# Kernel tuning notes

Measured on AMD Instinct MI355X. Metric: run time of the kernel, lower is better.

The kernel has to match this reference:

```python
import jax, jax.numpy as jnp
import numpy as np

N = 24  # input_size
TRIL = N * (N + 1) // 2  # 300
_rows, _cols = np.tril_indices(N)  # row-major order, matches torch.tril_indices


def setup_inputs() -> dict:
    key = jax.random.key(0)
    ks = jax.random.split(key, 8)
    B = 131072
    x = jax.random.normal(ks[0], (B, N), dtype=jnp.float32)
    # MLP params: Linear(N,128), Linear(128,32), Linear(32,TRIL)
    def lin(k, fan_in, fan_out):
        k1, k2 = jax.random.split(k)
        lim = 1.0 / np.sqrt(fan_in)
        W = jax.random.uniform(k1, (fan_out, fan_in), jnp.float32, -lim, lim)
        b = jax.random.uniform(k2, (fan_out,), jnp.float32, -lim, lim)
        return W, b
    W1, b1 = lin(ks[1], N, 128)
    W2, b2 = lin(ks[2], 128, 32)
    W3, b3 = lin(ks[3], 32, TRIL)
    return {"x": x, "W1": W1, "b1": b1, "W2": W2, "b2": b2, "W3": W3, "b3": b3}


def reference(x, W1, b1, W2, b2, W3, b3):
    # MLP: Linear -> ELU -> Linear -> ELU -> Linear -> Softplus
    h = jax.nn.elu(x @ W1.T + b1)           # [B,128]
    h = jax.nn.elu(h @ W2.T + b2)           # [B,32]
    c = jax.nn.softplus(h @ W3.T + b3)      # [B,TRIL]
    B = x.shape[0]
    # scatter into lower-triangular Cholesky factor
    L = jnp.zeros((B, N, N), dtype=x.dtype).at[:, _rows, _cols].set(c)  # [B,N,N]
    A = jnp.einsum('bij,bkj->bik', L, L)    # C @ C^T, SPD
    y = jnp.einsum('bi,bij,bj->b', x, A, x)[:, None]  # quadratic form, [B,1]
    return y
```

## Files before the change

### kernel.cpp

```cpp
#include <hip/hip_runtime.h>
#include <hip/hip_bf16.h>
#include <math.h>


constexpr int NI  = 24;
constexpr int H1  = 128;
constexpr int H2  = 32;
constexpr int SPB = 128;
constexpr int NT_TOT = 19;
constexpr int W3R = 304;
constexpr float LOG2E = 1.4426950408889634f;
constexpr float LN2SQ = 0.4804530139182014f;

typedef __attribute__((ext_vector_type(8))) short bf16x8;
typedef __attribute__((ext_vector_type(4))) float f32x4;

__device__ __forceinline__ float elu_f(float v) {
    return v > 0.0f ? v : __expf(v) - 1.0f;
}
__device__ __forceinline__ float exp2_hw(float x) {
    float r; asm("v_exp_f32 %0, %1" : "=v"(r) : "v"(x)); return r;
}
__device__ __forceinline__ float log2_hw(float x) {
    float r; asm("v_log_f32 %0, %1" : "=v"(r) : "v"(x)); return r;
}
__device__ __forceinline__ float softplus_g(float zp) {
    return fmaxf(zp, 0.0f) + log2_hw(1.0f + exp2_hw(-fabsf(zp)));
}
__device__ __forceinline__ unsigned short f2bf(float f) {
    return __builtin_bit_cast(unsigned short, __float2bfloat16(f));
}
__device__ __forceinline__ unsigned int pk2(float a, float b) {
    return (unsigned int)f2bf(a) | ((unsigned int)f2bf(b) << 16);
}

__global__ void wcvt(const float* __restrict__ W1, const float* __restrict__ W2,
                     const float* __restrict__ W3, const float* __restrict__ b3,
                     unsigned short* __restrict__ ws) {
    int idx = blockIdx.x * 256 + threadIdx.x;
    if (idx < 4096) {
        int n = idx >> 5, k = idx & 31;
        ws[idx] = f2bf(k < NI ? W1[n * NI + k] : 0.0f);
    } else if (idx < 8192) {
        ws[idx] = f2bf(W2[idx - 4096]);
    } else if (idx < 8192 + W3R * H2) {
        int j = idx - 8192;
        int t = j >> 5;
        ws[idx] = f2bf(t < 300 ? W3[j] * LOG2E : 0.0f);
    } else if (idx < 8192 + W3R * H2 + W3R) {
        int t = idx - (8192 + W3R * H2);
        float* b3s = reinterpret_cast<float*>(ws + 17920);
        b3s[t] = (t < 300) ? b3[t] * LOG2E : 0.0f;
    }
}

template<int J0, int C0>
__device__ __forceinline__ void vaccum(const float xr[NI], float v[12],
                                       const float* __restrict__ crow) {
    #pragma unroll
    for (int q = 0; q < 12; ++q) {
        const int j = 2 * q + J0;
        #pragma unroll
        for (int i = j; i < NI; ++i) {
            const int t = i * (i + 1) / 2 + j;
            if (t >= C0 && t < C0 + 32)
                v[q] = fmaf(xr[i], crow[t - C0], v[q]);
        }
    }
}

template<int CH>
__device__ __forceinline__ void chunk_body(
    int w_hi, int w_lo, int lr, int lq, int sid, int half,
    const unsigned short* __restrict__ w3b, const float* __restrict__ b3s,
    const float xr[NI], float v[12],
    float* __restrict__ c_buf, const unsigned short* __restrict__ h2b)
{
    const int my_nt = 2 * CH + w_hi;
    if (my_nt < NT_TOT) {
        const int t = my_nt * 16 + lr;
        bf16x8 wf = *reinterpret_cast<const bf16x8*>(w3b + t * H2 + lq * 8);
        const float bias = b3s[t];
        #pragma unroll
        for (int q = 0; q < 4; ++q) {
            const int st = 4 * w_lo + q;
            bf16x8 hb = *reinterpret_cast<const bf16x8*>(h2b + (st * 16 + lr) * 40 + lq * 8);
            f32x4 a = {0.f, 0.f, 0.f, 0.f};
            a = __builtin_amdgcn_mfma_f32_16x16x32_bf16(hb, wf, a, 0, 0, 0);
            #pragma unroll
            for (int r = 0; r < 4; ++r) {
                float g = softplus_g(a[r] + bias);
                c_buf[(st * 16 + 4 * lq + r) * 33 + (my_nt & 1) * 16 + lr] = g;
            }
        }
    }
    __syncthreads();
    if (half == 0) vaccum<1, CH * 32>(xr, v, c_buf + sid * 33);
    else           vaccum<0, CH * 32>(xr, v, c_buf + sid * 33);
    __syncthreads();
}

__global__ __launch_bounds__(256, 4) void qnet_fused(
    const float* __restrict__ x,
    const unsigned short* __restrict__ w1b, const float* __restrict__ b1,
    const unsigned short* __restrict__ w2b, const float* __restrict__ b2,
    const unsigned short* __restrict__ w3b, const float* __restrict__ b3s,
    float* __restrict__ y, int B)
{
    __shared__ __align__(16) unsigned char L[30720];
    unsigned short* xb  = reinterpret_cast<unsigned short*>(L);
    unsigned short* h1s = reinterpret_cast<unsigned short*>(L + 10240);
    unsigned short* h2b = reinterpret_cast<unsigned short*>(L + 20480);
    float* c_buf = reinterpret_cast<float*>(L);
    float* yb    = reinterpret_cast<float*>(L + 16896);

    const int tid  = threadIdx.x;
    const int sid  = tid & (SPB - 1);
    const int lane = tid & 63;
    const int lr   = lane & 15, lq = lane >> 4;
    const int half = __builtin_amdgcn_readfirstlane(tid >> 7);
    const int wid  = __builtin_amdgcn_readfirstlane(tid >> 6);
    const int w_hi = wid >> 1, w_lo = wid & 1;
    const size_t sbase = (size_t)blockIdx.x * SPB;

    float xr[NI];
    {
        const float4* xp4 = reinterpret_cast<const float4*>(x + (sbase + sid) * NI);
        #pragma unroll
        for (int q = 0; q < NI / 4; ++q) {
            float4 t4 = xp4[q];
            xr[4*q+0] = t4.x; xr[4*q+1] = t4.y; xr[4*q+2] = t4.z; xr[4*q+3] = t4.w;
        }
    }
    if (half == 0) {
        unsigned int pk[12];
        #pragma unroll
        for (int q = 0; q < 12; ++q) pk[q] = pk2(xr[2*q], xr[2*q+1]);
        uint4* dst = reinterpret_cast<uint4*>(xb + sid * 40);
        dst[0] = make_uint4(pk[0], pk[1], pk[2], pk[3]);
        dst[1] = make_uint4(pk[4], pk[5], pk[6], pk[7]);
        dst[2] = make_uint4(pk[8], pk[9], pk[10], pk[11]);
    } else {
        *reinterpret_cast<uint4*>(xb + sid * 40 + 24) = make_uint4(0, 0, 0, 0);
    }
    __syncthreads();

    f32x4 acc[2][2];
    #pragma unroll
    for (int u = 0; u < 2; ++u)
        #pragma unroll
        for (int n2 = 0; n2 < 2; ++n2) acc[u][n2] = (f32x4){0.f, 0.f, 0.f, 0.f};

    #pragma unroll
    for (int kk = 0; kk < 4; ++kk) {
        const int nt1 = 2 * kk + w_hi;
        bf16x8 af = *reinterpret_cast<const bf16x8*>(w1b + (nt1 * 16 + lr) * 32 + lq * 8);
        const float4 bb1 = *reinterpret_cast<const float4*>(b1 + nt1 * 16 + 4 * lq);
        #pragma unroll
        for (int q = 0; q < 4; ++q) {
            const int st = 4 * w_lo + q;
            bf16x8 bf = *reinterpret_cast<const bf16x8*>(xb + (st * 16 + lr) * 40 + lq * 8);
            f32x4 a = {0.f, 0.f, 0.f, 0.f};
            a = __builtin_amdgcn_mfma_f32_16x16x32_bf16(af, bf, a, 0, 0, 0);
            unsigned int p0 = pk2(elu_f(a[0] + bb1.x), elu_f(a[1] + bb1.y));
            unsigned int p1 = pk2(elu_f(a[2] + bb1.z), elu_f(a[3] + bb1.w));
            unsigned long long pw = (unsigned long long)p0 | ((unsigned long long)p1 << 32);
            *reinterpret_cast<unsigned long long*>(
                h1s + (st * 16 + lr) * 40 + w_hi * 16 + 4 * lq) = pw;
        }
        __syncthreads();
        #pragma unroll
        for (int u = 0; u < 2; ++u) {
            const int st2 = 2 * wid + u;
            bf16x8 hb = *reinterpret_cast<const bf16x8*>(h1s + (st2 * 16 + lr) * 40 + lq * 8);
            #pragma unroll
            for (int n2 = 0; n2 < 2; ++n2) {
                bf16x8 wf = *reinterpret_cast<const bf16x8*>(
                    w2b + (n2 * 16 + lr) * H1 + kk * 32 + lq * 8);
                acc[u][n2] = __builtin_amdgcn_mfma_f32_16x16x32_bf16(wf, hb, acc[u][n2], 0, 0, 0);
            }
        }
        __syncthreads();
    }

    #pragma unroll
    for (int u = 0; u < 2; ++u) {
        const int st2 = 2 * wid + u;
        #pragma unroll
        for (int n2 = 0; n2 < 2; ++n2) {
            const float4 bb2 = *reinterpret_cast<const float4*>(b2 + n2 * 16 + 4 * lq);
            unsigned int p0 = pk2(elu_f(acc[u][n2][0] + bb2.x), elu_f(acc[u][n2][1] + bb2.y));
            unsigned int p1 = pk2(elu_f(acc[u][n2][2] + bb2.z), elu_f(acc[u][n2][3] + bb2.w));
            unsigned long long pw = (unsigned long long)p0 | ((unsigned long long)p1 << 32);
            *reinterpret_cast<unsigned long long*>(
                h2b + (st2 * 16 + lr) * 40 + n2 * 16 + 4 * lq) = pw;
        }
    }
    __syncthreads();

    float v[12];
    #pragma unroll
    for (int q = 0; q < 12; ++q) v[q] = 0.f;

    chunk_body<0>(w_hi, w_lo, lr, lq, sid, half, w3b, b3s, xr, v, c_buf, h2b);
    chunk_body<1>(w_hi, w_lo, lr, lq, sid, half, w3b, b3s, xr, v, c_buf, h2b);
    chunk_body<2>(w_hi, w_lo, lr, lq, sid, half, w3b, b3s, xr, v, c_buf, h2b);
    chunk_body<3>(w_hi, w_lo, lr, lq, sid, half, w3b, b3s, xr, v, c_buf, h2b);
    chunk_body<4>(w_hi, w_lo, lr, lq, sid, half, w3b, b3s, xr, v, c_buf, h2b);
    chunk_body<5>(w_hi, w_lo, lr, lq, sid, half, w3b, b3s, xr, v, c_buf, h2b);
    chunk_body<6>(w_hi, w_lo, lr, lq, sid, half, w3b, b3s, xr, v, c_buf, h2b);
    chunk_body<7>(w_hi, w_lo, lr, lq, sid, half, w3b, b3s, xr, v, c_buf, h2b);
    chunk_body<8>(w_hi, w_lo, lr, lq, sid, half, w3b, b3s, xr, v, c_buf, h2b);
    chunk_body<9>(w_hi, w_lo, lr, lq, sid, half, w3b, b3s, xr, v, c_buf, h2b);

    float acc_y = 0.f;
    #pragma unroll
    for (int q = 0; q < 12; ++q) acc_y = fmaf(v[q], v[q], acc_y);

    if (half == 1) yb[sid] = acc_y;
    __syncthreads();
    if (half == 0) y[sbase + sid] = LN2SQ * (acc_y + yb[sid]);
}

extern "C" void kernel_launch(void* const* d_in, const int* in_sizes, int n_in,
                              void* d_out, int out_size, void* d_ws, size_t ws_size,
                              hipStream_t stream) {
    const float* x  = (const float*)d_in[0];
    const float* W1 = (const float*)d_in[1];
    const float* b1 = (const float*)d_in[2];
    const float* W2 = (const float*)d_in[3];
    const float* b2 = (const float*)d_in[4];
    const float* W3 = (const float*)d_in[5];
    const float* b3 = (const float*)d_in[6];
    float* y = (float*)d_out;

    unsigned short* ws = (unsigned short*)d_ws;
    const unsigned short* w1b = ws;
    const unsigned short* w2b = ws + 4096;
    const unsigned short* w3b = ws + 8192;
    const float* b3s = reinterpret_cast<const float*>(ws + 17920);

    const int B = in_sizes[0] / NI;
    const int cvt_elems = 8192 + W3R * H2 + W3R;
    wcvt<<<dim3((cvt_elems + 255) / 256), dim3(256), 0, stream>>>(W1, W2, W3, b3, ws);
    qnet_fused<<<dim3(B / SPB), dim3(256), 0, stream>>>(
        x, w1b, b1, w2b, b2, w3b, b3s, y, B);
}
```

Baseline: 35.62 us.

## Split triangle consumption by element halves and vectorize c_buf stores and loads

Swaps the MFMA operand order so each lane holds four consecutive triangle outputs, which can be written to LDS as one 16-byte vector into a row stride of 36 instead of four scalar stores at stride 33. The two thread halves now split each 32-entry chunk by element (16 each) rather than by odd/even column j. Each half keeps a full 24-wide v accumulator, and the halves combine the vectors through LDS before squaring. This aims to cut LDS instruction count and balance the FMA work between halves, at the cost of more registers for v and a larger final reduction exchange.

Measured after the change: 38.70 us. 8.7% more time.

```diff
diff --git a/kernel.cpp b/kernel.cpp
--- a/kernel.cpp
+++ b/kernel.cpp
@@ -14,6 +14,17 @@
 
 typedef __attribute__((ext_vector_type(8))) short bf16x8;
 typedef __attribute__((ext_vector_type(4))) float f32x4;
+
+struct TriMap { unsigned char i[320]; unsigned char j[320]; };
+constexpr TriMap mk_map() {
+    TriMap m{};
+    int t = 0;
+    for (int i = 0; i < NI; ++i)
+        for (int j = 0; j <= i; ++j) { m.i[t] = (unsigned char)i; m.j[t] = (unsigned char)j; ++t; }
+    for (; t < 320; ++t) { m.i[t] = 0; m.j[t] = 0; }
+    return m;
+}
+constexpr TriMap TM = mk_map();
 
 __device__ __forceinline__ float elu_f(float v) {
     return v > 0.0f ? v : __expf(v) - 1.0f;
@@ -54,49 +65,53 @@
     }
 }
 
-template<int J0, int C0>
-__device__ __forceinline__ void vaccum(const float xr[NI], float v[12],
-                                       const float* __restrict__ crow) {
-    #pragma unroll
-    for (int q = 0; q < 12; ++q) {
-        const int j = 2 * q + J0;
-        #pragma unroll
-        for (int i = j; i < NI; ++i) {
-            const int t = i * (i + 1) / 2 + j;
-            if (t >= C0 && t < C0 + 32)
-                v[q] = fmaf(xr[i], crow[t - C0], v[q]);
+template<int CH, int HF>
+__device__ __forceinline__ void consume3(const float* __restrict__ crow,
+                                         const float xr[NI], float v[NI]) {
+    constexpr int T0 = CH * 32 + HF * 16;
+    if constexpr (T0 < 300) {
+        const f32x4* p = reinterpret_cast<const f32x4*>(crow + HF * 16);
+        f32x4 cc[4];
+        cc[0] = p[0]; cc[1] = p[1]; cc[2] = p[2]; cc[3] = p[3];
+        #pragma unroll
+        for (int tl = 0; tl < 16; ++tl) {
+            if (T0 + tl < 300)
+                v[TM.j[T0 + tl]] =
+                    fmaf(xr[TM.i[T0 + tl]], cc[tl >> 2][tl & 3], v[TM.j[T0 + tl]]);
         }
     }
 }
 
 template<int CH>
-__device__ __forceinline__ void chunk_body(
+__device__ __forceinline__ void chunk3(
     int w_hi, int w_lo, int lr, int lq, int sid, int half,
     const unsigned short* __restrict__ w3b, const float* __restrict__ b3s,
-    const float xr[NI], float v[12],
+    const float xr[NI], float v[NI],
     float* __restrict__ c_buf, const unsigned short* __restrict__ h2b)
 {
     const int my_nt = 2 * CH + w_hi;
     if (my_nt < NT_TOT) {
-        const int t = my_nt * 16 + lr;
-        bf16x8 wf = *reinterpret_cast<const bf16x8*>(w3b + t * H2 + lq * 8);
-        const float bias = b3s[t];
+        const int trow = my_nt * 16;
+        bf16x8 af = *reinterpret_cast<const bf16x8*>(w3b + (trow + lr) * H2 + lq * 8);
+        const float4 b4 = *reinterpret_cast<const float4*>(b3s + trow + 4 * lq);
         #pragma unroll
         for (int q = 0; q < 4; ++q) {
             const int st = 4 * w_lo + q;
             bf16x8 hb = *reinterpret_cast<const bf16x8*>(h2b + (st * 16 + lr) * 40 + lq * 8);
             f32x4 a = {0.f, 0.f, 0.f, 0.f};
-            a = __builtin_amdgcn_mfma_f32_16x16x32_bf16(hb, wf, a, 0, 0, 0);
-            #pragma unroll
-            for (int r = 0; r < 4; ++r) {
-                float g = softplus_g(a[r] + bias);
-                c_buf[(st * 16 + 4 * lq + r) * 33 + (my_nt & 1) * 16 + lr] = g;
-            }
-        }
-    }
-    __syncthreads();
-    if (half == 0) vaccum<1, CH * 32>(xr, v, c_buf + sid * 33);
-    else           vaccum<0, CH * 32>(xr, v, c_buf + sid * 33);
+            a = __builtin_amdgcn_mfma_f32_16x16x32_bf16(af, hb, a, 0, 0, 0);
+            f32x4 w;
+            w[0] = softplus_g(a[0] + b4.x);
+            w[1] = softplus_g(a[1] + b4.y);
+            w[2] = softplus_g(a[2] + b4.z);
+            w[3] = softplus_g(a[3] + b4.w);
+            *reinterpret_cast<f32x4*>(
+                c_buf + (st * 16 + lr) * 36 + (my_nt & 1) * 16 + 4 * lq) = w;
+        }
+    }
+    __syncthreads();
+    if (half == 0) consume3<CH, 0>(c_buf + sid * 36, xr, v);
+    else           consume3<CH, 1>(c_buf + sid * 36, xr, v);
     __syncthreads();
 }
 
@@ -112,7 +127,6 @@
     unsigned short* h1s = reinterpret_cast<unsigned short*>(L + 10240);
     unsigned short* h2b = reinterpret_cast<unsigned short*>(L + 20480);
     float* c_buf = reinterpret_cast<float*>(L);
-    float* yb    = reinterpret_cast<float*>(L + 16896);
 
     const int tid  = threadIdx.x;
     const int sid  = tid & (SPB - 1);
@@ -198,28 +212,45 @@
     }
     __syncthreads();
 
-    float v[12];
-    #pragma unroll
-    for (int q = 0; q < 12; ++q) v[q] = 0.f;
-
-    chunk_body<0>(w_hi, w_lo, lr, lq, sid, half, w3b, b3s, xr, v, c_buf, h2b);
-    chunk_body<1>(w_hi, w_lo, lr, lq, sid, half, w3b, b3s, xr, v, c_buf, h2b);
-    chunk_body<2>(w_hi, w_lo, lr, lq, sid, half, w3b, b3s, xr, v, c_buf, h2b);
-    chunk_body<3>(w_hi, w_lo, lr, lq, sid, half, w3b, b3s, xr, v, c_buf, h2b);
-    chunk_body<4>(w_hi, w_lo, lr, lq, sid, half, w3b, b3s, xr, v, c_buf, h2b);
-    chunk_body<5>(w_hi, w_lo, lr, lq, sid, half, w3b, b3s, xr, v, c_buf, h2b);
-    chunk_body<6>(w_hi, w_lo, lr, lq, sid, half, w3b, b3s, xr, v, c_buf, h2b);
-    chunk_body<7>(w_hi, w_lo, lr, lq, sid, half, w3b, b3s, xr, v, c_buf, h2b);
-    chunk_body<8>(w_hi, w_lo, lr, lq, sid, half, w3b, b3s, xr, v, c_buf, h2b);
-    chunk_body<9>(w_hi, w_lo, lr, lq, sid, half, w3b, b3s, xr, v, c_buf, h2b);
-
-    float acc_y = 0.f;
-    #pragma unroll
-    for (int q = 0; q < 12; ++q) acc_y = fmaf(v[q], v[q], acc_y);
-
-    if (half == 1) yb[sid] = acc_y;
-    __syncthreads();
-    if (half == 0) y[sbase + sid] = LN2SQ * (acc_y + yb[sid]);
+    float v[NI];
+    #pragma unroll
+    for (int q = 0; q < NI; ++q) v[q] = 0.f;
+
+    chunk3<0>(w_hi, w_lo, lr, lq, sid, half, w3b, b3s, xr, v, c_buf, h2b);
+    chunk3<1>(w_hi, w_lo, lr, lq, sid, half, w3b, b3s, xr, v, c_buf, h2b);
+    chunk3<2>(w_hi, w_lo, lr, lq, sid, half, w3b, b3s, xr, v, c_buf, h2b);
+    chunk3<3>(w_hi, w_lo, lr, lq, sid, half, w3b, b3s, xr, v, c_buf, h2b);
+    chunk3<4>(w_hi, w_lo, lr, lq, sid, half, w3b, b3s, xr, v, c_buf, h2b);
+    chunk3<5>(w_hi, w_lo, lr, lq, sid, half, w3b, b3s, xr, v, c_buf, h2b);
+    chunk3<6>(w_hi, w_lo, lr, lq, sid, half, w3b, b3s, xr, v, c_buf, h2b);
+    chunk3<7>(w_hi, w_lo, lr, lq, sid, half, w3b, b3s, xr, v, c_buf, h2b);
+    chunk3<8>(w_hi, w_lo, lr, lq, sid, half, w3b, b3s, xr, v, c_buf, h2b);
+    chunk3<9>(w_hi, w_lo, lr, lq, sid, half, w3b, b3s, xr, v, c_buf, h2b);
+
+    float* vx = c_buf;
+    if (half == 1) {
+        f32x4* dst = reinterpret_cast<f32x4*>(vx + sid * 24);
+        #pragma unroll
+        for (int q = 0; q < 6; ++q) {
+            f32x4 t4 = { v[4*q], v[4*q+1], v[4*q+2], v[4*q+3] };
+            dst[q] = t4;
+        }
+    }
+    __syncthreads();
+    if (half == 0) {
+        const f32x4* src = reinterpret_cast<const f32x4*>(vx + sid * 24);
+        float acc_y = 0.f;
+        #pragma unroll
+        for (int q = 0; q < 6; ++q) {
+            f32x4 t4 = src[q];
+            #pragma unroll
+            for (int r = 0; r < 4; ++r) {
+                float sv = v[4*q + r] + t4[r];
+                acc_y = fmaf(sv, sv, acc_y);
+            }
+        }
+        y[sbase + sid] = LN2SQ * acc_y;
+    }
 }
 
 extern "C" void kernel_launch(void* const* d_in, const int* in_sizes, int n_in,
```

## Restructure fused MLP so each wave owns its samples and splits quadratic-form work

Applied to the files above, without the earlier changes.

Halves samples per block to 64. Each wave now loads its own 16-sample x fragment straight into bf16 MFMA registers and runs layers 1 and 2 without block-wide barriers. Layer-3 softplus outputs go to shared memory as packed bf16 in a parity double buffer, so each chunk needs one barrier instead of two. The four waves split the Cholesky column accumulation by column class, using a constexpr triangle index map. Shared memory is smaller so launch bounds can target 8 blocks per CU, at the cost of storing the Cholesky entries in bf16 and adding a final cross-wave reduction through shared memory.

New measurement: 41.13 us. 1.15x slower.

```diff
diff --git a/kernel.cpp b/kernel.cpp
--- a/kernel.cpp
+++ b/kernel.cpp
@@ -6,7 +6,7 @@
 constexpr int NI  = 24;
 constexpr int H1  = 128;
 constexpr int H2  = 32;
-constexpr int SPB = 128;
+constexpr int SPB = 64;
 constexpr int NT_TOT = 19;
 constexpr int W3R = 304;
 constexpr float LOG2E = 1.4426950408889634f;
@@ -15,6 +15,17 @@
 typedef __attribute__((ext_vector_type(8))) short bf16x8;
 typedef __attribute__((ext_vector_type(4))) float f32x4;
 
+struct TriMap { unsigned char i[320]; unsigned char j[320]; };
+constexpr TriMap mk_map() {
+    TriMap m{};
+    int t = 0;
+    for (int i = 0; i < NI; ++i)
+        for (int j = 0; j <= i; ++j) { m.i[t] = (unsigned char)i; m.j[t] = (unsigned char)j; ++t; }
+    for (; t < 320; ++t) { m.i[t] = 0; m.j[t] = 0; }
+    return m;
+}
+constexpr TriMap TM = mk_map();
+
 __device__ __forceinline__ float elu_f(float v) {
     return v > 0.0f ? v : __expf(v) - 1.0f;
 }
@@ -32,6 +43,12 @@
 }
 __device__ __forceinline__ unsigned int pk2(float a, float b) {
     return (unsigned int)f2bf(a) | ((unsigned int)f2bf(b) << 16);
+}
+__device__ __forceinline__ bf16x8 cvt8(const float* __restrict__ p) {
+    float4 a = *reinterpret_cast<const float4*>(p);
+    float4 b = *reinterpret_cast<const float4*>(p + 4);
+    uint4 u = make_uint4(pk2(a.x, a.y), pk2(a.z, a.w), pk2(b.x, b.y), pk2(b.z, b.w));
+    return __builtin_bit_cast(bf16x8, u);
 }
 
 __global__ void wcvt(const float* __restrict__ W1, const float* __restrict__ W2,
@@ -54,172 +71,152 @@
     }
 }
 
-template<int J0, int C0>
-__device__ __forceinline__ void vaccum(const float xr[NI], float v[12],
-                                       const float* __restrict__ crow) {
-    #pragma unroll
-    for (int q = 0; q < 12; ++q) {
-        const int j = 2 * q + J0;
-        #pragma unroll
-        for (int i = j; i < NI; ++i) {
-            const int t = i * (i + 1) / 2 + j;
-            if (t >= C0 && t < C0 + 32)
-                v[q] = fmaf(xr[i], crow[t - C0], v[q]);
-        }
-    }
-}
-
-template<int CH>
-__device__ __forceinline__ void chunk_body(
-    int w_hi, int w_lo, int lr, int lq, int sid, int half,
-    const unsigned short* __restrict__ w3b, const float* __restrict__ b3s,
-    const float xr[NI], float v[12],
-    float* __restrict__ c_buf, const unsigned short* __restrict__ h2b)
-{
-    const int my_nt = 2 * CH + w_hi;
-    if (my_nt < NT_TOT) {
-        const int t = my_nt * 16 + lr;
-        bf16x8 wf = *reinterpret_cast<const bf16x8*>(w3b + t * H2 + lq * 8);
-        const float bias = b3s[t];
-        #pragma unroll
-        for (int q = 0; q < 4; ++q) {
-            const int st = 4 * w_lo + q;
-            bf16x8 hb = *reinterpret_cast<const bf16x8*>(h2b + (st * 16 + lr) * 40 + lq * 8);
-            f32x4 a = {0.f, 0.f, 0.f, 0.f};
-            a = __builtin_amdgcn_mfma_f32_16x16x32_bf16(hb, wf, a, 0, 0, 0);
-            #pragma unroll
-            for (int r = 0; r < 4; ++r) {
-                float g = softplus_g(a[r] + bias);
-                c_buf[(st * 16 + 4 * lq + r) * 33 + (my_nt & 1) * 16 + lr] = g;
+
+template<int CH, int W>
+__device__ __forceinline__ void consume4(const unsigned int* __restrict__ crow,
+                                         const float xr[NI], float v[6]) {
+    #pragma unroll
+    for (int tl = 0; tl < 32; ++tl) {
+        const int t = CH * 32 + tl;
+        if (t < 300) {
+            const int j = TM.j[t];
+            if ((j & 7) == W || (j & 7) == (7 - W)) {
+                const int slot = 2 * (j >> 3) + (((j & 7) == W) ? 0 : 1);
+                unsigned int u = crow[(CH & 1) * 16 + (tl >> 1)];
+                unsigned int bits = (tl & 1) ? (u & 0xffff0000u) : (u << 16);
+                float cv = __builtin_bit_cast(float, bits);
+                v[slot] = fmaf(xr[TM.i[t]], cv, v[slot]);
             }
         }
     }
-    __syncthreads();
-    if (half == 0) vaccum<1, CH * 32>(xr, v, c_buf + sid * 33);
-    else           vaccum<0, CH * 32>(xr, v, c_buf + sid * 33);
-    __syncthreads();
-}
-
-__global__ __launch_bounds__(256, 4) void qnet_fused(
+}
+
+__global__ __launch_bounds__(256, 8) void qnet_fused(
     const float* __restrict__ x,
     const unsigned short* __restrict__ w1b, const float* __restrict__ b1,
     const unsigned short* __restrict__ w2b, const float* __restrict__ b2,
     const unsigned short* __restrict__ w3b, const float* __restrict__ b3s,
     float* __restrict__ y, int B)
 {
-    __shared__ __align__(16) unsigned char L[30720];
-    unsigned short* xb  = reinterpret_cast<unsigned short*>(L);
-    unsigned short* h1s = reinterpret_cast<unsigned short*>(L + 10240);
-    unsigned short* h2b = reinterpret_cast<unsigned short*>(L + 20480);
-    float* c_buf = reinterpret_cast<float*>(L);
-    float* yb    = reinterpret_cast<float*>(L + 16896);
+    __shared__ __align__(16) unsigned char L[15104];
+    unsigned short* h2b = reinterpret_cast<unsigned short*>(L);
+    unsigned short* h1s = reinterpret_cast<unsigned short*>(L + 5120);
+    unsigned int*   cbw = reinterpret_cast<unsigned int*>(L + 5120);
+    float*          vx  = reinterpret_cast<float*>(L + 5120);
 
     const int tid  = threadIdx.x;
-    const int sid  = tid & (SPB - 1);
     const int lane = tid & 63;
     const int lr   = lane & 15, lq = lane >> 4;
-    const int half = __builtin_amdgcn_readfirstlane(tid >> 7);
-    const int wid  = __builtin_amdgcn_readfirstlane(tid >> 6);
-    const int w_hi = wid >> 1, w_lo = wid & 1;
+    const int w    = __builtin_amdgcn_readfirstlane(tid >> 6);
     const size_t sbase = (size_t)blockIdx.x * SPB;
 
     float xr[NI];
     {
-        const float4* xp4 = reinterpret_cast<const float4*>(x + (sbase + sid) * NI);
+        const float4* xp4 = reinterpret_cast<const float4*>(x + (sbase + lane) * NI);
         #pragma unroll
         for (int q = 0; q < NI / 4; ++q) {
             float4 t4 = xp4[q];
             xr[4*q+0] = t4.x; xr[4*q+1] = t4.y; xr[4*q+2] = t4.z; xr[4*q+3] = t4.w;
         }
     }
-    if (half == 0) {
-        unsigned int pk[12];
+
+    const int srow = w * 16 + lr;
+    bf16x8 xf = cvt8(x + (sbase + srow) * NI + (lq == 3 ? 0 : lq * 8));
+
+    f32x4 acc[2];
+    acc[0] = (f32x4){0.f, 0.f, 0.f, 0.f};
+    acc[1] = (f32x4){0.f, 0.f, 0.f, 0.f};
+
+    #pragma unroll
+    for (int kk = 0; kk < 4; ++kk) {
         #pragma unroll
-        for (int q = 0; q < 12; ++q) pk[q] = pk2(xr[2*q], xr[2*q+1]);
-        uint4* dst = reinterpret_cast<uint4*>(xb + sid * 40);
-        dst[0] = make_uint4(pk[0], pk[1], pk[2], pk[3]);
-        dst[1] = make_uint4(pk[4], pk[5], pk[6], pk[7]);
-        dst[2] = make_uint4(pk[8], pk[9], pk[10], pk[11]);
-    } else {
-        *reinterpret_cast<uint4*>(xb + sid * 40 + 24) = make_uint4(0, 0, 0, 0);
-    }
-    __syncthreads();
-
-    f32x4 acc[2][2];
-    #pragma unroll
-    for (int u = 0; u < 2; ++u)
-        #pragma unroll
-        for (int n2 = 0; n2 < 2; ++n2) acc[u][n2] = (f32x4){0.f, 0.f, 0.f, 0.f};
-
-    #pragma unroll
-    for (int kk = 0; kk < 4; ++kk) {
-        const int nt1 = 2 * kk + w_hi;
-        bf16x8 af = *reinterpret_cast<const bf16x8*>(w1b + (nt1 * 16 + lr) * 32 + lq * 8);
-        const float4 bb1 = *reinterpret_cast<const float4*>(b1 + nt1 * 16 + 4 * lq);
-        #pragma unroll
-        for (int q = 0; q < 4; ++q) {
-            const int st = 4 * w_lo + q;
-            bf16x8 bf = *reinterpret_cast<const bf16x8*>(xb + (st * 16 + lr) * 40 + lq * 8);
+        for (int n = 0; n < 2; ++n) {
+            const int nt1 = 2 * kk + n;
+            bf16x8 af = *reinterpret_cast<const bf16x8*>(w1b + (nt1 * 16 + lr) * 32 + lq * 8);
+            const float4 bb1 = *reinterpret_cast<const float4*>(b1 + nt1 * 16 + 4 * lq);
             f32x4 a = {0.f, 0.f, 0.f, 0.f};
-            a = __builtin_amdgcn_mfma_f32_16x16x32_bf16(af, bf, a, 0, 0, 0);
+            a = __builtin_amdgcn_mfma_f32_16x16x32_bf16(af, xf, a, 0, 0, 0);
             unsigned int p0 = pk2(elu_f(a[0] + bb1.x), elu_f(a[1] + bb1.y));
             unsigned int p1 = pk2(elu_f(a[2] + bb1.z), elu_f(a[3] + bb1.w));
             unsigned long long pw = (unsigned long long)p0 | ((unsigned long long)p1 << 32);
             *reinterpret_cast<unsigned long long*>(
-                h1s + (st * 16 + lr) * 40 + w_hi * 16 + 4 * lq) = pw;
-        }
-        __syncthreads();
-        #pragma unroll
-        for (int u = 0; u < 2; ++u) {
-            const int st2 = 2 * wid + u;
-            bf16x8 hb = *reinterpret_cast<const bf16x8*>(h1s + (st2 * 16 + lr) * 40 + lq * 8);
-            #pragma unroll
-            for (int n2 = 0; n2 < 2; ++n2) {
-                bf16x8 wf = *reinterpret_cast<const bf16x8*>(
-                    w2b + (n2 * 16 + lr) * H1 + kk * 32 + lq * 8);
-                acc[u][n2] = __builtin_amdgcn_mfma_f32_16x16x32_bf16(wf, hb, acc[u][n2], 0, 0, 0);
-            }
-        }
-        __syncthreads();
-    }
-
-    #pragma unroll
-    for (int u = 0; u < 2; ++u) {
-        const int st2 = 2 * wid + u;
+                h1s + srow * 40 + n * 16 + 4 * lq) = pw;
+        }
+        bf16x8 hb = *reinterpret_cast<const bf16x8*>(h1s + srow * 40 + lq * 8);
         #pragma unroll
         for (int n2 = 0; n2 < 2; ++n2) {
-            const float4 bb2 = *reinterpret_cast<const float4*>(b2 + n2 * 16 + 4 * lq);
-            unsigned int p0 = pk2(elu_f(acc[u][n2][0] + bb2.x), elu_f(acc[u][n2][1] + bb2.y));
-            unsigned int p1 = pk2(elu_f(acc[u][n2][2] + bb2.z), elu_f(acc[u][n2][3] + bb2.w));
-            unsigned long long pw = (unsigned long long)p0 | ((unsigned long long)p1 << 32);
-            *reinterpret_cast<unsigned long long*>(
-                h2b + (st2 * 16 + lr) * 40 + n2 * 16 + 4 * lq) = pw;
-        }
+            bf16x8 wf = *reinterpret_cast<const bf16x8*>(
+                w2b + (n2 * 16 + lr) * H1 + kk * 32 + lq * 8);
+            acc[n2] = __builtin_amdgcn_mfma_f32_16x16x32_bf16(wf, hb, acc[n2], 0, 0, 0);
+        }
+    }
+
+    #pragma unroll
+    for (int n2 = 0; n2 < 2; ++n2) {
+        const float4 bb2 = *reinterpret_cast<const float4*>(b2 + n2 * 16 + 4 * lq);
+        unsigned int p0 = pk2(elu_f(acc[n2][0] + bb2.x), elu_f(acc[n2][1] + bb2.y));
+        unsigned int p1 = pk2(elu_f(acc[n2][2] + bb2.z), elu_f(acc[n2][3] + bb2.w));
+        unsigned long long pw = (unsigned long long)p0 | ((unsigned long long)p1 << 32);
+        *reinterpret_cast<unsigned long long*>(
+            h2b + srow * 40 + n2 * 16 + 4 * lq) = pw;
     }
     __syncthreads();
 
-    float v[12];
-    #pragma unroll
-    for (int q = 0; q < 12; ++q) v[q] = 0.f;
-
-    chunk_body<0>(w_hi, w_lo, lr, lq, sid, half, w3b, b3s, xr, v, c_buf, h2b);
-    chunk_body<1>(w_hi, w_lo, lr, lq, sid, half, w3b, b3s, xr, v, c_buf, h2b);
-    chunk_body<2>(w_hi, w_lo, lr, lq, sid, half, w3b, b3s, xr, v, c_buf, h2b);
-    chunk_body<3>(w_hi, w_lo, lr, lq, sid, half, w3b, b3s, xr, v, c_buf, h2b);
-    chunk_body<4>(w_hi, w_lo, lr, lq, sid, half, w3b, b3s, xr, v, c_buf, h2b);
-    chunk_body<5>(w_hi, w_lo, lr, lq, sid, half, w3b, b3s, xr, v, c_buf, h2b);
-    chunk_body<6>(w_hi, w_lo, lr, lq, sid, half, w3b, b3s, xr, v, c_buf, h2b);
-    chunk_body<7>(w_hi, w_lo, lr, lq, sid, half, w3b, b3s, xr, v, c_buf, h2b);
-    chunk_body<8>(w_hi, w_lo, lr, lq, sid, half, w3b, b3s, xr, v, c_buf, h2b);
-    chunk_body<9>(w_hi, w_lo, lr, lq, sid, half, w3b, b3s, xr, v, c_buf, h2b);
-
-    float acc_y = 0.f;
-    #pragma unroll
-    for (int q = 0; q < 12; ++q) acc_y = fmaf(v[q], v[q], acc_y);
-
-    if (half == 1) yb[sid] = acc_y;
+    float v[6];
+    #pragma unroll
+    for (int q = 0; q < 6; ++q) v[q] = 0.f;
+
+    const int nt_off = w >> 1;
+    const int st0 = 2 * (w & 1);
+
+#define QNET_CHUNK(CH)                                                         \
+    {                                                                          \
+        const int my_nt = 2 * (CH) + nt_off;                                   \
+        if (my_nt < NT_TOT) {                                                  \
+            bf16x8 af = *reinterpret_cast<const bf16x8*>(                      \
+                w3b + (my_nt * 16 + lr) * H2 + lq * 8);                        \
+            const float4 b4 = *reinterpret_cast<const float4*>(                \
+                b3s + my_nt * 16 + 4 * lq);                                    \
+            _Pragma("unroll")                                                  \
+            for (int u = 0; u < 2; ++u) {                                      \
+                const int st = st0 + u;                                        \
+                bf16x8 hb = *reinterpret_cast<const bf16x8*>(                  \
+                    h2b + (st * 16 + lr) * 40 + lq * 8);                       \
+                f32x4 a = {0.f, 0.f, 0.f, 0.f};                                \
+                a = __builtin_amdgcn_mfma_f32_16x16x32_bf16(af, hb, a, 0, 0, 0);\
+                float s0 = softplus_g(a[0] + b4.x);                            \
+                float s1 = softplus_g(a[1] + b4.y);                            \
+                float s2 = softplus_g(a[2] + b4.z);                            \
+                float s3 = softplus_g(a[3] + b4.w);                            \
+                const int word = (st * 16 + lr) * 39 + ((CH) & 1) * 16         \
+                                 + nt_off * 8 + 2 * lq;                        \
+                cbw[word]     = pk2(s0, s1);                                   \
+                cbw[word + 1] = pk2(s2, s3);                                   \
+            }                                                                  \
+        }                                                                      \
+        __syncthreads();                                                       \
+        const unsigned int* crow = cbw + lane * 39;                            \
+        if      (w == 0) consume4<(CH), 0>(crow, xr, v);                       \
+        else if (w == 1) consume4<(CH), 1>(crow, xr, v);                       \
+        else if (w == 2) consume4<(CH), 2>(crow, xr, v);                       \
+        else             consume4<(CH), 3>(crow, xr, v);                       \
+    }
+
+    QNET_CHUNK(0) QNET_CHUNK(1) QNET_CHUNK(2) QNET_CHUNK(3) QNET_CHUNK(4)
+    QNET_CHUNK(5) QNET_CHUNK(6) QNET_CHUNK(7) QNET_CHUNK(8) QNET_CHUNK(9)
+#undef QNET_CHUNK
+
+    float py = 0.f;
+    #pragma unroll
+    for (int q = 0; q < 6; ++q) py = fmaf(v[q], v[q], py);
+
     __syncthreads();
-    if (half == 0) y[sbase + sid] = LN2SQ * (acc_y + yb[sid]);
+    if (w > 0) vx[lane * 4 + (w - 1)] = py;
+    __syncthreads();
+    if (w == 0) {
+        float tot = py + vx[lane * 4 + 0] + vx[lane * 4 + 1] + vx[lane * 4 + 2];
+        y[sbase + lane] = LN2SQ * tot;
+    }
 }
 
 extern "C" void kernel_launch(void* const* d_in, const int* in_sizes, int n_in,
```
